# Optimization experiments

Hardware: AMD Instinct MI355X
Metric: run time of the kernel (lower is better)

The kernel has to match this reference:

```python
import jax, jax.numpy as jnp
import numpy as np

ISQRT2 = 0.7071067811865476  # 1/sqrt(2), haar analysis/synthesis coefficient
LEVELS = 13                  # pywt.dwt_max_level(8192, 'haar') = log2(8192)
J = 4                        # recursion_limit
BN_EPS = 1e-5


def haar_wavedec(x, levels):
    """Full-depth haar DWT (mode='zero' is exact for power-of-2 length).
    x: [..., N]. Returns bank [cA_L, cD_L, cD_{L-1}, ..., cD_1] (pywt order).
    Vectorized over batch AND channel dims at once (the per-channel python
    loop in the torch module computes identical math per channel)."""
    a = x
    details = []
    for _ in range(levels):
        even, odd = a[..., ::2], a[..., 1::2]
        details.append((even - odd) * ISQRT2)
        a = (even + odd) * ISQRT2
    return [a] + details[::-1]


def haar_waverec(bank):
    """Inverse of haar_wavedec; bank in pywt order [cA, cD_coarse..cD_fine]."""
    a = bank[0]
    for d in bank[1:]:
        up = jnp.stack([a + d, a - d], axis=-1) * ISQRT2  # interleave even/odd
        a = up.reshape(a.shape[:-1] + (a.shape[-1] * 2,))
    return a


def batch_norm_train(y, g, b):
    # BatchNorm1d training mode: stats over (batch, length) per channel, biased var
    mean = jnp.mean(y, axis=(0, 2), keepdims=True)
    var = jnp.var(y, axis=(0, 2), keepdims=True)
    return (y - mean) * jax.lax.rsqrt(var + BN_EPS) * g[None, :, None] + b[None, :, None]


def reference(x, gamma, beta):
    # x: [B, C, N]; gamma, beta: [J, C]
    bank = haar_wavedec(x, LEVELS)  # computed once, reused for all masks
    zeros_bank = [jnp.zeros_like(c) for c in bank]

    # masked_inputs[j]: IWT keeping only band j (pool_inputs=False -> full bank)
    masked_inputs = []
    for j in range(J):
        mb = [bank[i] if i == j else zeros_bank[i] for i in range(len(bank))]
        masked_inputs.append(haar_waverec(mb))

    # masked_targets[j]: IWT keeping bands 0..j (pool_targets=False)
    masked_targets = []
    for j in range(J):
        mb = [bank[i] if i <= j else zeros_bank[i] for i in range(len(bank))]
        masked_targets.append(haar_waverec(mb))

    # per-level BatchNorm on inputs only
    masked_inputs = [batch_norm_train(masked_inputs[j], gamma[j], beta[j]) for j in range(J)]

    # stack for a single output tensor: [2, J, B, C, N]
    return jnp.stack([jnp.stack(masked_inputs), jnp.stack(masked_targets)])


def setup_inputs() -> dict:
    key = jax.random.key(0)
    x = jax.random.normal(key, (64, 16, 8192), dtype=jnp.float32)
    gamma = jnp.ones((J, 16), dtype=jnp.float32)
    beta = jnp.zeros((J, 16), dtype=jnp.float32)
    return {"x": x, "gamma": gamma, "beta": beta}
```

## Files before the change

### kernel.cpp

```cpp
#include <hip/hip_runtime.h>


#define STATS_STRIDE 16

typedef float f32x4 __attribute__((ext_vector_type(4)));

__global__ __launch_bounds__(256) void row_stats_kernel(const float* __restrict__ x,
                                                        float* __restrict__ stats) {
    int row = blockIdx.x;
    int t = threadIdx.x;
    int lane = t & 63, wave = t >> 6;
    const f32x4* xr = reinterpret_cast<const f32x4*>(x) + (size_t)row * 2048;
    float s[8];
#pragma unroll
    for (int k = 0; k < 8; ++k) {
        f32x4 v = __builtin_nontemporal_load(&xr[t + 256 * k]);
        s[k] = (v.x + v.y) + (v.z + v.w);
    }
    __shared__ float red[8][4];
    __shared__ float sb[16];
#pragma unroll
    for (int k = 0; k < 8; ++k) {
        float v = s[k];
#pragma unroll
        for (int off = 32; off; off >>= 1) v += __shfl_down(v, off, 64);
        if (lane == 0) red[k][wave] = v;
    }
    __syncthreads();
    if (t < 8) sb[7 + t] = (red[t][0] + red[t][1] + red[t][2] + red[t][3]) * (1.0f / 1024.0f);
    __syncthreads();
    if (t == 0) {
        float m2[4], m1[2];
#pragma unroll
        for (int k = 0; k < 4; ++k) m2[k] = 0.5f * (sb[7 + 2 * k] + sb[7 + 2 * k + 1]);
        m1[0] = 0.5f * (m2[0] + m2[1]);
        m1[1] = 0.5f * (m2[2] + m2[3]);
        sb[0] = 0.5f * (m1[0] + m1[1]);
        sb[1] = m1[0]; sb[2] = m1[1];
        sb[3] = m2[0]; sb[4] = m2[1]; sb[5] = m2[2]; sb[6] = m2[3];
    }
    __syncthreads();
    if (t < 15) stats[(size_t)row * STATS_STRIDE + t] = sb[t];
}

__global__ __launch_bounds__(256) void write_all_kernel(const float* __restrict__ stats,
                                                        const float* __restrict__ gamma,
                                                        const float* __restrict__ beta,
                                                        f32x4* __restrict__ out) {
    int row = blockIdx.x;
    int c = row & 15;
    int t = threadIdx.x;
    int lane = t & 63, wave = t >> 6;

    __shared__ float ss[4][2];
    {
        int j = wave;
        const float* sp = stats + (size_t)((lane << 4) + c) * STATS_STRIDE;
        float sum = 0.f, sum2 = 0.f;
        if (j == 0) {
            float d = sp[0];
            sum = d; sum2 = d * d;
        } else {
            int base = (1 << j) - 1, pb = (1 << (j - 1)) - 1;
            for (int k = 0; k < (1 << j); ++k) {
                float d = sp[base + k] - sp[pb + (k >> 1)];
                sum += d; sum2 += d * d;
            }
        }
        float B = (float)(8192 >> j);
        sum *= B; sum2 *= B;
#pragma unroll
        for (int off = 32; off; off >>= 1) {
            sum  += __shfl_down(sum, off, 64);
            sum2 += __shfl_down(sum2, off, 64);
        }
        if (lane == 0) {
            const float N = 64.0f * 8192.0f;
            float mean = sum / N;
            float var = sum2 / N - mean * mean;
            float inv = rsqrtf(var + 1e-5f);
            float sc = gamma[(j << 4) + c] * inv;
            ss[j][0] = sc;
            ss[j][1] = beta[(j << 4) + c] - mean * sc;
        }
    }
    float rv[15];
    {
        const float* sp = stats + (size_t)row * STATS_STRIDE;
#pragma unroll
        for (int k = 0; k < 15; ++k) rv[k] = sp[k];
    }
    __syncthreads();

#pragma unroll
    for (int j = 0; j < 4; ++j) {
        f32x4* orow = out + ((size_t)(4 + j) * 1024 + row) * 2048;
        int sh = 3 - j;
#pragma unroll
        for (int i = 0; i < 8; ++i) {
            float v = rv[(1 << j) - 1 + (i >> sh)];
            f32x4 q = {v, v, v, v};
            orow[t + (i << 8)] = q;
        }
    }
#pragma unroll
    for (int j = 0; j < 4; ++j) {
        float sc = ss[j][0], sh0 = ss[j][1];
        int shr = 3 - j;
        f32x4* orow = out + ((size_t)j * 1024 + row) * 2048;
#pragma unroll
        for (int i = 0; i < 8; ++i) {
            int run = i >> shr;
            float mj = rv[(1 << j) - 1 + run];
            float d = (j == 0) ? mj : mj - rv[(1 << (j - 1)) - 1 + (run >> 1)];
            float v = d * sc + sh0;
            f32x4 q = {v, v, v, v};
            orow[t + (i << 8)] = q;
        }
    }
}

extern "C" void kernel_launch(void* const* d_in, const int* in_sizes, int n_in,
                              void* d_out, int out_size, void* d_ws, size_t ws_size,
                              hipStream_t stream) {
    const float* x     = (const float*)d_in[0];
    const float* gamma = (const float*)d_in[1];
    const float* beta  = (const float*)d_in[2];
    f32x4* out = (f32x4*)d_out;
    float* stats = (float*)d_ws;

    row_stats_kernel<<<1024, 256, 0, stream>>>(x, stats);
    write_all_kernel<<<1024, 256, 0, stream>>>(stats, gamma, beta, out);
}
```

Measured before the change: 55.25 us.

## Precompute per-row band moments and remap write kernel to contiguous output blocks

The stats kernel now also writes per-row second moments for each band, so the write kernel no longer has to loop over band differences for every row when building BatchNorm statistics. The write kernel is remapped so each of 512 blocks owns one contiguous 512KB chunk of output (part, band, batch) and writes all 16 channels from a small shared value table. The nontemporal load on x is also dropped. The change cuts redundant reduction work and makes stores contiguous per block, but halves the block count and issues 128 stores per thread, which could lower occupancy and latency hiding.

```diff
diff --git a/kernel.cpp b/kernel.cpp
--- a/kernel.cpp
+++ b/kernel.cpp
@@ -1,12 +1,13 @@
 #include <hip/hip_runtime.h>
 
 
-#define STATS_STRIDE 16
+#define SSTR 16
 
 typedef float f32x4 __attribute__((ext_vector_type(4)));
 
 __global__ __launch_bounds__(256) void row_stats_kernel(const float* __restrict__ x,
-                                                        float* __restrict__ stats) {
+                                                        float* __restrict__ stats,
+                                                        float* __restrict__ mom) {
     int row = blockIdx.x;
     int t = threadIdx.x;
     int lane = t & 63, wave = t >> 6;
@@ -14,7 +15,7 @@
     float s[8];
 #pragma unroll
     for (int k = 0; k < 8; ++k) {
-        f32x4 v = __builtin_nontemporal_load(&xr[t + 256 * k]);
+        f32x4 v = xr[t + 256 * k];
         s[k] = (v.x + v.y) + (v.z + v.w);
     }
     __shared__ float red[8][4];
@@ -32,7 +33,7 @@
     if (t == 0) {
         float m2[4], m1[2];
 #pragma unroll
-        for (int k = 0; k < 4; ++k) m2[k] = 0.5f * (sb[7 + 2 * k] + sb[7 + 2 * k + 1]);
+        for (int k = 0; k < 4; ++k) m2[k] = 0.5f * (sb[7 + 2 * k] + sb[8 + 2 * k]);
         m1[0] = 0.5f * (m2[0] + m2[1]);
         m1[1] = 0.5f * (m2[2] + m2[3]);
         sb[0] = 0.5f * (m1[0] + m1[1]);
@@ -40,83 +41,96 @@
         sb[3] = m2[0]; sb[4] = m2[1]; sb[5] = m2[2]; sb[6] = m2[3];
     }
     __syncthreads();
-    if (t < 15) stats[(size_t)row * STATS_STRIDE + t] = sb[t];
+    if (t < 15) stats[(size_t)row * SSTR + t] = sb[t];
+    if (t < 4) {
+        int j = t, nb = 1 << j;
+        float acc;
+        if (j == 0) {
+            acc = sb[0] * sb[0];
+        } else {
+            int base = nb - 1, pb = (nb >> 1) - 1;
+            acc = 0.f;
+            for (int k = 0; k < nb; ++k) {
+                float d = sb[base + k] - sb[pb + (k >> 1)];
+                acc += d * d;
+            }
+        }
+        mom[(size_t)row * 4 + j] = acc * (float)(8192 >> j);
+    }
+}
+
+template <int JJ>
+__device__ inline void store_region(const float* __restrict__ val, f32x4* __restrict__ ob, int t) {
+#pragma unroll
+    for (int i = 0; i < 128; ++i) {
+        int c = i >> 3;
+        int run = (i & 7) >> (3 - JJ);
+        float v = val[c * 8 + run];
+        f32x4 q = {v, v, v, v};
+        ob[i * 256 + t] = q;
+    }
 }
 
 __global__ __launch_bounds__(256) void write_all_kernel(const float* __restrict__ stats,
+                                                        const float* __restrict__ mom,
                                                         const float* __restrict__ gamma,
                                                         const float* __restrict__ beta,
                                                         f32x4* __restrict__ out) {
-    int row = blockIdx.x;
-    int c = row & 15;
+    int blk = blockIdx.x;
+    int part = blk >> 8;
+    int j = (blk >> 6) & 3;
+    int b = blk & 63;
     int t = threadIdx.x;
     int lane = t & 63, wave = t >> 6;
+    int nb = 1 << j;
 
-    __shared__ float ss[4][2];
-    {
-        int j = wave;
-        const float* sp = stats + (size_t)((lane << 4) + c) * STATS_STRIDE;
-        float sum = 0.f, sum2 = 0.f;
-        if (j == 0) {
-            float d = sp[0];
-            sum = d; sum2 = d * d;
-        } else {
-            int base = (1 << j) - 1, pb = (1 << (j - 1)) - 1;
-            for (int k = 0; k < (1 << j); ++k) {
-                float d = sp[base + k] - sp[pb + (k >> 1)];
-                sum += d; sum2 += d * d;
+    __shared__ float sc[16], sh[16];
+    __shared__ float val[128];
+
+    if (part == 0) {
+#pragma unroll
+        for (int q = 0; q < 4; ++q) {
+            int c = wave * 4 + q;
+            float m = mom[((size_t)(lane << 4) + c) * 4 + j];
+            float mu = (j == 0) ? stats[((size_t)(lane << 4) + c) * SSTR] : 0.f;
+#pragma unroll
+            for (int off = 32; off; off >>= 1) {
+                m  += __shfl_down(m, off, 64);
+                mu += __shfl_down(mu, off, 64);
+            }
+            if (lane == 0) {
+                const float N = 64.0f * 8192.0f;
+                float mean = mu * (1.0f / 64.0f);
+                float var = m / N - mean * mean;
+                float s_ = gamma[(j << 4) + c] * rsqrtf(var + 1e-5f);
+                sc[c] = s_;
+                sh[c] = beta[(j << 4) + c] - mean * s_;
             }
         }
-        float B = (float)(8192 >> j);
-        sum *= B; sum2 *= B;
-#pragma unroll
-        for (int off = 32; off; off >>= 1) {
-            sum  += __shfl_down(sum, off, 64);
-            sum2 += __shfl_down(sum2, off, 64);
+    }
+    __syncthreads();
+    if (t < 128) {
+        int c = t >> 3, run = t & 7;
+        int rr = run & (nb - 1);
+        const float* sp = stats + ((size_t)(b << 4) + c) * SSTR;
+        float m = sp[nb - 1 + rr];
+        float v;
+        if (part) {
+            v = m;
+        } else {
+            float d = (j == 0) ? m : m - sp[(nb >> 1) - 1 + (rr >> 1)];
+            v = d * sc[c] + sh[c];
         }
-        if (lane == 0) {
-            const float N = 64.0f * 8192.0f;
-            float mean = sum / N;
-            float var = sum2 / N - mean * mean;
-            float inv = rsqrtf(var + 1e-5f);
-            float sc = gamma[(j << 4) + c] * inv;
-            ss[j][0] = sc;
-            ss[j][1] = beta[(j << 4) + c] - mean * sc;
-        }
-    }
-    float rv[15];
-    {
-        const float* sp = stats + (size_t)row * STATS_STRIDE;
-#pragma unroll
-        for (int k = 0; k < 15; ++k) rv[k] = sp[k];
+        val[t] = v;
     }
     __syncthreads();
 
-#pragma unroll
-    for (int j = 0; j < 4; ++j) {
-        f32x4* orow = out + ((size_t)(4 + j) * 1024 + row) * 2048;
-        int sh = 3 - j;
-#pragma unroll
-        for (int i = 0; i < 8; ++i) {
-            float v = rv[(1 << j) - 1 + (i >> sh)];
-            f32x4 q = {v, v, v, v};
-            orow[t + (i << 8)] = q;
-        }
-    }
-#pragma unroll
-    for (int j = 0; j < 4; ++j) {
-        float sc = ss[j][0], sh0 = ss[j][1];
-        int shr = 3 - j;
-        f32x4* orow = out + ((size_t)j * 1024 + row) * 2048;
-#pragma unroll
-        for (int i = 0; i < 8; ++i) {
-            int run = i >> shr;
-            float mj = rv[(1 << j) - 1 + run];
-            float d = (j == 0) ? mj : mj - rv[(1 << (j - 1)) - 1 + (run >> 1)];
-            float v = d * sc + sh0;
-            f32x4 q = {v, v, v, v};
-            orow[t + (i << 8)] = q;
-        }
+    f32x4* ob = out + (size_t)blk * 32768;
+    switch (j) {
+        case 0: store_region<0>(val, ob, t); break;
+        case 1: store_region<1>(val, ob, t); break;
+        case 2: store_region<2>(val, ob, t); break;
+        default: store_region<3>(val, ob, t); break;
     }
 }
 
@@ -128,7 +142,8 @@
     const float* beta  = (const float*)d_in[2];
     f32x4* out = (f32x4*)d_out;
     float* stats = (float*)d_ws;
+    float* mom   = stats + (size_t)1024 * SSTR;
 
-    row_stats_kernel<<<1024, 256, 0, stream>>>(x, stats);
-    write_all_kernel<<<1024, 256, 0, stream>>>(stats, gamma, beta, out);
+    row_stats_kernel<<<1024, 256, 0, stream>>>(x, stats, mom);
+    write_all_kernel<<<512, 256, 0, stream>>>(stats, mom, gamma, beta, out);
 }
```

Result: slower. 60.45 us (+9.4%).
